# Kernel tuning notes

Hardware: AMD Instinct MI355X
Metric: run time of the kernel (lower is better)

The kernel has to match this reference:

```python
import jax, jax.numpy as jnp
import numpy as np

D_MODEL = 1024
NUM_HEADS = 16
D_K = D_MODEL // NUM_HEADS


def setup_inputs() -> dict:
    key = jax.random.key(0)
    ks = jax.random.split(key, 11)
    B, T = 4, 2048
    s = 1.0 / np.sqrt(D_MODEL)
    return {
        'query': jax.random.normal(ks[0], (B, T, D_MODEL), jnp.float32),
        'key': jax.random.normal(ks[1], (B, T, D_MODEL), jnp.float32),
        'value': jax.random.normal(ks[2], (B, T, D_MODEL), jnp.float32),
        'Wq': jax.random.normal(ks[3], (D_MODEL, D_MODEL), jnp.float32) * s,
        'bq': jnp.zeros((D_MODEL,), jnp.float32),
        'Wk': jax.random.normal(ks[4], (D_MODEL, D_MODEL), jnp.float32) * s,
        'bk': jnp.zeros((D_MODEL,), jnp.float32),
        'Wv': jax.random.normal(ks[5], (D_MODEL, D_MODEL), jnp.float32) * s,
        'bv': jnp.zeros((D_MODEL,), jnp.float32),
        'Wo': jax.random.normal(ks[6], (D_MODEL, D_MODEL), jnp.float32) * s,
        'bo': jnp.zeros((D_MODEL,), jnp.float32),
    }


def reference(query, key, value, Wq, bq, Wk, bk, Wv, bv, Wo, bo):
    B, Tq, _ = query.shape
    Tk = key.shape[1]
    # projections (torch Linear: x @ W.T + b)
    q = (query @ Wq.T + bq).reshape(B, Tq, NUM_HEADS, D_K).transpose(0, 2, 1, 3)
    k = (key @ Wk.T + bk).reshape(B, Tk, NUM_HEADS, D_K).transpose(0, 2, 1, 3)
    v = (value @ Wv.T + bv).reshape(B, Tk, NUM_HEADS, D_K).transpose(0, 2, 1, 3)
    scale = 1.0 / jnp.sqrt(jnp.asarray(D_K, q.dtype))
    scores = jnp.einsum('bhqd,bhkd->bhqk', q, k) * scale  # [B,H,Tq,Tk]
    attn = jax.nn.softmax(scores, axis=-1)
    out = jnp.einsum('bhqk,bhkd->bhqd', attn, v)
    out = out.transpose(0, 2, 1, 3).reshape(B, Tq, D_MODEL)
    return out @ Wo.T + bo
```

## Files before the change

kernel.cpp:

```cpp
#include <hip/hip_runtime.h>

typedef unsigned short u16;
typedef unsigned int u32;
typedef __attribute__((ext_vector_type(8))) short bf16x8;
typedef __attribute__((ext_vector_type(4))) float f32x4;

__device__ inline u16 f2bf(float x) {
  union { float f; unsigned u; } v; v.f = x;
  unsigned r = v.u + 0x7fffu + ((v.u >> 16) & 1u);
  return (u16)(r >> 16);
}

__device__ inline u32 packbf2(float p0, float p1) {
  return __builtin_amdgcn_perm(__float_as_uint(p1), __float_as_uint(p0), 0x07060302u);
}

__device__ inline void gload16(const void* g, void* l) {
  __builtin_amdgcn_global_load_lds(
      (const __attribute__((address_space(1))) unsigned int*)g,
      (__attribute__((address_space(3))) unsigned int*)l,
      16, 0, 0);
}

__global__ void cvt_all(const float* __restrict__ q, const float* __restrict__ k,
                        const float* __restrict__ v,
                        const float* __restrict__ wq, const float* __restrict__ wk,
                        const float* __restrict__ wv, const float* __restrict__ wo,
                        u16* __restrict__ ws) {
  const size_t MT4 = (size_t)2 * 1024 * 1024;
  const int i = blockIdx.x * blockDim.x + threadIdx.x;
  const int t = blockIdx.y;
  float4 vv;
  ushort4 o;
  if (t < 3) {
    const float* src = (t == 0) ? q : (t == 1) ? k : v;
    vv = ((const float4*)src)[i];
    o.x = f2bf(vv.x); o.y = f2bf(vv.y); o.z = f2bf(vv.z); o.w = f2bf(vv.w);
    ((ushort4*)ws)[(size_t)t * MT4 + i] = o;
  } else {
    if (i >= (1 << 20)) return;
    const int w = i >> 18, j = i & 0x3FFFF;
    const float* src = (w == 0) ? wq : (w == 1) ? wk : (w == 2) ? wv : wo;
    vv = ((const float4*)src)[j];
    o.x = f2bf(vv.x); o.y = f2bf(vv.y); o.z = f2bf(vv.z); o.w = f2bf(vv.w);
    ((ushort4*)(ws + 3 * MT4 * 4))[i] = o;
  }
}

__global__ __launch_bounds__(512, 4) void gemm_qkv(
    const u16* __restrict__ Xq, const u16* __restrict__ Wqb,
    const float* __restrict__ bq_, const float* __restrict__ bk_,
    const float* __restrict__ bv_, u16* __restrict__ Qp)
{
  constexpr int N = 1024, K = 1024, BK = 32, NT = K / BK;
  constexpr size_t MT = (size_t)8192 * 1024, WT = (size_t)1024 * 1024;
  __shared__ __align__(16) u16 As[3][128 * BK];
  __shared__ __align__(16) u16 Bs[3][128 * BK];
  const int z = blockIdx.z;
  const u16* A = Xq + (size_t)z * MT;
  const u16* W = Wqb + (size_t)z * WT;
  const float* bias = (z == 0) ? bq_ : (z == 1) ? bk_ : bv_;
  u16* Cout = Qp + (size_t)z * MT;
  const bool vm = (z == 2);

  const int tid = threadIdx.x;
  const int wave = tid >> 6, lane = tid & 63;
  const int quad = lane >> 4, l16 = lane & 15;
  const int m0 = blockIdx.x * 128, n0 = blockIdx.y * 128;

  const int srow = tid >> 2;
  const int sg = ((tid & 3) ^ (srow & 3)) * 8;
  const int arowP = vm ? ((srow & 64) + (srow & 3) * 16 + ((srow & 63) >> 2)) : srow;
  const u16* ag = A + (size_t)(m0 + arowP) * K + sg;
  const u16* bg = W + (size_t)(n0 + srow) * K + sg;

  const int wm = (wave >> 2) * 64, wn = (wave & 3) * 32;
  f32x4 acc[4][2] = {};

#define QKV_STAGE(s)                                   \
  do {                                                 \
    gload16(ag, As[s] + wave * 512);                   \
    gload16(bg, Bs[s] + wave * 512);                   \
    ag += BK; bg += BK;                                \
  } while (0)

  QKV_STAGE(0);
  QKV_STAGE(1);

  int cb = 0, sb = 2;
  for (int kt = 0; kt < NT; ++kt) {
    if (kt + 1 < NT) asm volatile("s_waitcnt vmcnt(2)" ::: "memory");
    else             asm volatile("s_waitcnt vmcnt(0)" ::: "memory");
    __builtin_amdgcn_s_barrier();
    __builtin_amdgcn_sched_barrier(0);
    if (kt + 2 < NT) {
      QKV_STAGE(sb);
      sb = (sb == 2) ? 0 : sb + 1;
    }
    const u16* Ac = As[cb];
    const u16* Bc = Bs[cb];
    cb = (cb == 2) ? 0 : cb + 1;
    bf16x8 af[4], bf[2];
#pragma unroll
    for (int mi = 0; mi < 4; ++mi)
      af[mi] = *(const bf16x8*)(Ac + (wm + mi * 16 + l16) * BK + ((quad ^ (l16 & 3)) * 8));
#pragma unroll
    for (int ni = 0; ni < 2; ++ni)
      bf[ni] = *(const bf16x8*)(Bc + (wn + ni * 16 + l16) * BK + ((quad ^ (l16 & 3)) * 8));
#pragma unroll
    for (int mi = 0; mi < 4; ++mi)
#pragma unroll
      for (int ni = 0; ni < 2; ++ni)
        acc[mi][ni] = __builtin_amdgcn_mfma_f32_16x16x32_bf16(af[mi], bf[ni], acc[mi][ni], 0, 0, 0);
  }
#undef QKV_STAGE

#pragma unroll
  for (int ni = 0; ni < 2; ++ni) {
    const int col = n0 + wn + ni * 16 + l16;
    const float bv = bias[col];
#pragma unroll
    for (int mi = 0; mi < 4; ++mi) {
      const int mrow = m0 + wm + mi * 16 + quad * 4;
      f32x4 a = acc[mi][ni];
      if (!vm) {
#pragma unroll
        for (int r = 0; r < 4; ++r)
          Cout[(size_t)(mrow + r) * N + col] = f2bf(a[r] + bv);
      } else {
        const int bq = mrow >> 11, t = mrow & 2047;
        const int h = col >> 6, d = col & 63;
        ushort4 pk;
        pk.x = f2bf(a[0] + bv); pk.y = f2bf(a[1] + bv);
        pk.z = f2bf(a[2] + bv); pk.w = f2bf(a[3] + bv);
        *(ushort4*)(Cout + ((size_t)((bq * 16 + h) * 64 + d)) * 2048 + t) = pk;
      }
    }
  }
}

__global__ __launch_bounds__(512, 4) void gemm_wo(
    const u16* __restrict__ A, const u16* __restrict__ W,
    const float* __restrict__ bias, float* __restrict__ Cout)
{
  constexpr int N = 1024, K = 1024, BK = 32, NT = K / BK;
  __shared__ __align__(16) u16 As[3][128 * BK];
  __shared__ __align__(16) u16 Bs[3][128 * BK];
  const int tid = threadIdx.x;
  const int wave = tid >> 6, lane = tid & 63;
  const int quad = lane >> 4, l16 = lane & 15;
  const int m0 = blockIdx.x * 128, n0 = blockIdx.y * 128;

  const int srow = tid >> 2;
  const int sg = ((tid & 3) ^ (srow & 3)) * 8;
  const u16* ag = A + (size_t)(m0 + srow) * K + sg;
  const u16* bg = W + (size_t)(n0 + srow) * K + sg;

  const int wm = (wave >> 2) * 64, wn = (wave & 3) * 32;
  f32x4 acc[4][2] = {};

#define WO_STAGE(s)                                    \
  do {                                                 \
    gload16(ag, As[s] + wave * 512);                   \
    gload16(bg, Bs[s] + wave * 512);                   \
    ag += BK; bg += BK;                                \
  } while (0)

  WO_STAGE(0);
  WO_STAGE(1);

  int cb = 0, sb = 2;
  for (int kt = 0; kt < NT; ++kt) {
    if (kt + 1 < NT) asm volatile("s_waitcnt vmcnt(2)" ::: "memory");
    else             asm volatile("s_waitcnt vmcnt(0)" ::: "memory");
    __builtin_amdgcn_s_barrier();
    __builtin_amdgcn_sched_barrier(0);
    if (kt + 2 < NT) {
      WO_STAGE(sb);
      sb = (sb == 2) ? 0 : sb + 1;
    }
    const u16* Ac = As[cb];
    const u16* Bc = Bs[cb];
    cb = (cb == 2) ? 0 : cb + 1;
    bf16x8 af[4], bf[2];
#pragma unroll
    for (int mi = 0; mi < 4; ++mi)
      af[mi] = *(const bf16x8*)(Ac + (wm + mi * 16 + l16) * BK + ((quad ^ (l16 & 3)) * 8));
#pragma unroll
    for (int ni = 0; ni < 2; ++ni)
      bf[ni] = *(const bf16x8*)(Bc + (wn + ni * 16 + l16) * BK + ((quad ^ (l16 & 3)) * 8));
#pragma unroll
    for (int mi = 0; mi < 4; ++mi)
#pragma unroll
      for (int ni = 0; ni < 2; ++ni)
        acc[mi][ni] = __builtin_amdgcn_mfma_f32_16x16x32_bf16(af[mi], bf[ni], acc[mi][ni], 0, 0, 0);
  }
#undef WO_STAGE

#pragma unroll
  for (int ni = 0; ni < 2; ++ni) {
    const int col = n0 + wn + ni * 16 + l16;
    const float bv = bias[col];
#pragma unroll
    for (int mi = 0; mi < 4; ++mi) {
      const int mrow = m0 + wm + mi * 16 + quad * 4;
      f32x4 a = acc[mi][ni];
#pragma unroll
      for (int r = 0; r < 4; ++r)
        Cout[(size_t)(mrow + r) * N + col] = a[r] + bv;
    }
  }
}

__global__ __launch_bounds__(512, 4) void flash_attn(
    const u16* __restrict__ Qp, const u16* __restrict__ Kp,
    const u16* __restrict__ Vt, u16* __restrict__ Ctx)
{
  constexpr int TQ = 2048, DM = 1024, DK = 64;
  __shared__ __align__(16) u16 Ks[2][128 * 64];
  __shared__ __align__(16) u16 Vts[2][64 * 128];
  __shared__ __align__(16) u16 Ps[8][16 * 64];

  const int bh = blockIdx.x, b = bh >> 4, h = bh & 15;
  const int qt = blockIdx.y;
  const int tid = threadIdx.x, wave = tid >> 6, lane = tid & 63;
  const int quad = lane >> 4, l16 = lane & 15;
  const int q0 = qt * 256 + wave * 32;

  const int C0 = tid, C1 = 512 + tid;
  const int kr0 = C0 >> 3, kr1 = C1 >> 3;
  const u16* kp0 = Kp + (size_t)(b * TQ + kr0) * DM + h * DK + (((C0 & 7) ^ (kr0 & 7)) * 8);
  const u16* kp1 = Kp + (size_t)(b * TQ + kr1) * DM + h * DK + (((C1 & 7) ^ (kr1 & 7)) * 8);
  const int vd0 = C0 >> 4, vd1 = C1 >> 4;
  const u16* vp0 = Vt + (size_t)(bh * DK + vd0) * TQ + (((C0 & 15) ^ (vd0 & 15)) * 8);
  const u16* vp1 = Vt + (size_t)(bh * DK + vd1) * TQ + (((C1 & 15) ^ (vd1 & 15)) * 8);

  bf16x8 qf[2][2];
#pragma unroll
  for (int mi = 0; mi < 2; ++mi)
#pragma unroll
    for (int ks = 0; ks < 2; ++ks)
      qf[mi][ks] = *(const bf16x8*)(Qp + (size_t)(b * TQ + q0 + mi * 16 + l16) * DM
                                       + h * DK + ks * 32 + quad * 8);

  f32x4 O[2][4] = {};
  f32x4 lsum[2] = {};
  const float CS = 0.18033688011112042f;
  const float CB = 0.0028153f;

  bf16x8 onesv;
#pragma unroll
  for (int j = 0; j < 8; ++j) onesv[j] = (short)0x3F80;

  gload16(kp0, &Ks[0][C0 * 8]);
  gload16(kp1, &Ks[0][C1 * 8]);
  gload16(vp0, &Vts[0][C0 * 8]);
  gload16(vp1, &Vts[0][C1 * 8]);
  kp0 += 128 * DM; kp1 += 128 * DM; vp0 += 128; vp1 += 128;
  __syncthreads();

  const int kg = quad ^ (l16 & 7);
  int cur = 0;
  for (int kt = 0; kt < TQ / 128; ++kt) {
    if (kt + 1 < TQ / 128) {
      const int nb = cur ^ 1;
      gload16(kp0, &Ks[nb][C0 * 8]);
      gload16(kp1, &Ks[nb][C1 * 8]);
      gload16(vp0, &Vts[nb][C0 * 8]);
      gload16(vp1, &Vts[nb][C1 * 8]);
      kp0 += 128 * DM; kp1 += 128 * DM; vp0 += 128; vp1 += 128;
    }
    const u16* Kc = Ks[cur];
    const u16* Vc = Vts[cur];
    u16* Psw = Ps[wave];

#pragma unroll
    for (int g = 0; g < 2; ++g) {
      f32x4 Sg[2][4];
      __builtin_amdgcn_s_setprio(1);
#pragma unroll
      for (int cc = 0; cc < 4; ++cc) {
        const int row = (g * 4 + cc) * 16 + l16;
        bf16x8 kf0 = *(const bf16x8*)(Kc + row * 64 + kg * 8);
        bf16x8 kf1 = *(const bf16x8*)(Kc + row * 64 + (kg ^ 4) * 8);
#pragma unroll
        for (int mi = 0; mi < 2; ++mi) {
          f32x4 zz = {};
          zz = __builtin_amdgcn_mfma_f32_16x16x32_bf16(qf[mi][0], kf0, zz, 0, 0, 0);
          Sg[mi][cc] = __builtin_amdgcn_mfma_f32_16x16x32_bf16(qf[mi][1], kf1, zz, 0, 0, 0);
        }
      }
      __builtin_amdgcn_s_setprio(0);
      bf16x8 pf[2][2];
#pragma unroll
      for (int mi = 0; mi < 2; ++mi) {
#pragma unroll
        for (int r = 0; r < 4; ++r) {
          float e0 = __builtin_amdgcn_exp2f(fmaf(Sg[mi][0][r], CS, CB));
          float e1 = __builtin_amdgcn_exp2f(fmaf(Sg[mi][1][r], CS, CB));
          float e2 = __builtin_amdgcn_exp2f(fmaf(Sg[mi][2][r], CS, CB));
          float e3 = __builtin_amdgcn_exp2f(fmaf(Sg[mi][3][r], CS, CB));
          uint2 pk;
          pk.x = packbf2(e0, e1);
          pk.y = packbf2(e2, e3);
          const int pw = quad * 4 + r;
          *(uint2*)(&Psw[pw * 64 + ((l16 * 4) ^ ((pw & 7) << 3))]) = pk;
        }
#pragma unroll
        for (int ksl = 0; ksl < 2; ++ksl)
          pf[mi][ksl] = *(const bf16x8*)(&Psw[l16 * 64 + ((ksl * 32 + quad * 8) ^ ((l16 & 7) << 3))]);
#pragma unroll
        for (int ksl = 0; ksl < 2; ++ksl)
          lsum[mi] = __builtin_amdgcn_mfma_f32_16x16x32_bf16(pf[mi][ksl], onesv, lsum[mi], 0, 0, 0);
      }
      __builtin_amdgcn_s_setprio(1);
#pragma unroll
      for (int ksl = 0; ksl < 2; ++ksl)
#pragma unroll
        for (int ni = 0; ni < 4; ++ni) {
          const int gv = g * 8 + ksl * 4 + quad;
          bf16x8 vf = *(const bf16x8*)(Vc + (ni * 16 + l16) * 128 + ((gv ^ l16) * 8));
          O[0][ni] = __builtin_amdgcn_mfma_f32_16x16x32_bf16(pf[0][ksl], vf, O[0][ni], 0, 0, 0);
          O[1][ni] = __builtin_amdgcn_mfma_f32_16x16x32_bf16(pf[1][ksl], vf, O[1][ni], 0, 0, 0);
        }
      __builtin_amdgcn_s_setprio(0);
    }
    __syncthreads();
    cur ^= 1;
  }

#pragma unroll
  for (int mi = 0; mi < 2; ++mi)
#pragma unroll
    for (int r = 0; r < 4; ++r) {
      const float inv = 1.0f / lsum[mi][r];
      const int q = q0 + mi * 16 + quad * 4 + r;
#pragma unroll
      for (int ni = 0; ni < 4; ++ni) {
        const int col = h * DK + ni * 16 + l16;
        Ctx[(size_t)(b * TQ + q) * DM + col] = f2bf(O[mi][ni][r] * inv);
      }
    }
}

extern "C" void kernel_launch(void* const* d_in, const int* in_sizes, int n_in,
                              void* d_out, int out_size, void* d_ws, size_t ws_size,
                              hipStream_t stream)
{
  (void)in_sizes; (void)n_in; (void)out_size; (void)ws_size;
  const float* query = (const float*)d_in[0];
  const float* key_  = (const float*)d_in[1];
  const float* value = (const float*)d_in[2];
  const float* Wq = (const float*)d_in[3];
  const float* bq = (const float*)d_in[4];
  const float* Wk = (const float*)d_in[5];
  const float* bk = (const float*)d_in[6];
  const float* Wv = (const float*)d_in[7];
  const float* bv = (const float*)d_in[8];
  const float* Wo = (const float*)d_in[9];
  const float* bo = (const float*)d_in[10];

  const size_t MT = (size_t)4 * 2048 * 1024;
  const size_t WT = (size_t)1024 * 1024;
  u16* ws  = (u16*)d_ws;
  u16* Xq  = ws;
  u16* Wqb = Xq + 3 * MT;
  u16* Qp  = Wqb + 4 * WT;
  u16* Kp  = Qp + MT;
  u16* Vt  = Kp + MT;
  u16* Ctx = Vt + MT;
  u16* Wob = Wqb + 3 * WT;

  cvt_all<<<dim3(8192, 4), 256, 0, stream>>>(
      query, key_, value, Wq, Wk, Wv, Wo, ws);

  gemm_qkv<<<dim3(64, 8, 3), 512, 0, stream>>>(Xq, Wqb, bq, bk, bv, Qp);

  flash_attn<<<dim3(64, 8), 512, 0, stream>>>(Qp, Kp, Vt, Ctx);

  gemm_wo<<<dim3(64, 8), 512, 0, stream>>>(Ctx, Wob, bo, (float*)d_out);
}
```

Before: 325.0 us.

## Keep softmax probabilities in registers by computing transposed QK^T scores

```diff
diff --git a/kernel.cpp b/kernel.cpp
--- a/kernel.cpp
+++ b/kernel.cpp
@@ -70,7 +70,8 @@
 
   const int srow = tid >> 2;
   const int sg = ((tid & 3) ^ (srow & 3)) * 8;
-  const int arowP = vm ? ((srow & 64) + (srow & 3) * 16 + ((srow & 63) >> 2)) : srow;
+  const int arowP = vm ? ((srow & ~31) | ((srow & 4) << 2) | ((srow & 24) >> 1) | (srow & 3))
+                       : srow;
   const u16* ag = A + (size_t)(m0 + arowP) * K + sg;
   const u16* bg = W + (size_t)(n0 + srow) * K + sg;
 
@@ -219,7 +220,6 @@
   constexpr int TQ = 2048, DM = 1024, DK = 64;
   __shared__ __align__(16) u16 Ks[2][128 * 64];
   __shared__ __align__(16) u16 Vts[2][64 * 128];
-  __shared__ __align__(16) u16 Ps[8][16 * 64];
 
   const int bh = blockIdx.x, b = bh >> 4, h = bh & 15;
   const int qt = blockIdx.y;
@@ -272,7 +272,6 @@
     }
     const u16* Kc = Ks[cur];
     const u16* Vc = Vts[cur];
-    u16* Psw = Ps[wave];
 
 #pragma unroll
     for (int g = 0; g < 2; ++g) {
@@ -286,32 +285,29 @@
 #pragma unroll
         for (int mi = 0; mi < 2; ++mi) {
           f32x4 zz = {};
-          zz = __builtin_amdgcn_mfma_f32_16x16x32_bf16(qf[mi][0], kf0, zz, 0, 0, 0);
-          Sg[mi][cc] = __builtin_amdgcn_mfma_f32_16x16x32_bf16(qf[mi][1], kf1, zz, 0, 0, 0);
+          zz = __builtin_amdgcn_mfma_f32_16x16x32_bf16(kf0, qf[mi][0], zz, 0, 0, 0);
+          Sg[mi][cc] = __builtin_amdgcn_mfma_f32_16x16x32_bf16(kf1, qf[mi][1], zz, 0, 0, 0);
         }
       }
       __builtin_amdgcn_s_setprio(0);
-      bf16x8 pf[2][2];
+      bf16x8 pa[2][2];
 #pragma unroll
       for (int mi = 0; mi < 2; ++mi) {
 #pragma unroll
-        for (int r = 0; r < 4; ++r) {
-          float e0 = __builtin_amdgcn_exp2f(fmaf(Sg[mi][0][r], CS, CB));
-          float e1 = __builtin_amdgcn_exp2f(fmaf(Sg[mi][1][r], CS, CB));
-          float e2 = __builtin_amdgcn_exp2f(fmaf(Sg[mi][2][r], CS, CB));
-          float e3 = __builtin_amdgcn_exp2f(fmaf(Sg[mi][3][r], CS, CB));
-          uint2 pk;
-          pk.x = packbf2(e0, e1);
-          pk.y = packbf2(e2, e3);
-          const int pw = quad * 4 + r;
-          *(uint2*)(&Psw[pw * 64 + ((l16 * 4) ^ ((pw & 7) << 3))]) = pk;
+        for (int ksl = 0; ksl < 2; ++ksl) {
+          uint4 u;
+          u.x = packbf2(__builtin_amdgcn_exp2f(fmaf(Sg[mi][2 * ksl][0], CS, CB)),
+                        __builtin_amdgcn_exp2f(fmaf(Sg[mi][2 * ksl][1], CS, CB)));
+          u.y = packbf2(__builtin_amdgcn_exp2f(fmaf(Sg[mi][2 * ksl][2], CS, CB)),
+                        __builtin_amdgcn_exp2f(fmaf(Sg[mi][2 * ksl][3], CS, CB)));
+          u.z = packbf2(__builtin_amdgcn_exp2f(fmaf(Sg[mi][2 * ksl + 1][0], CS, CB)),
+                        __builtin_amdgcn_exp2f(fmaf(Sg[mi][2 * ksl + 1][1], CS, CB)));
+          u.w = packbf2(__builtin_amdgcn_exp2f(fmaf(Sg[mi][2 * ksl + 1][2], CS, CB)),
+                        __builtin_amdgcn_exp2f(fmaf(Sg[mi][2 * ksl + 1][3], CS, CB)));
+          pa[mi][ksl] = *(const bf16x8*)&u;
         }
-#pragma unroll
-        for (int ksl = 0; ksl < 2; ++ksl)
-          pf[mi][ksl] = *(const bf16x8*)(&Psw[l16 * 64 + ((ksl * 32 + quad * 8) ^ ((l16 & 7) << 3))]);
-#pragma unroll
-        for (int ksl = 0; ksl < 2; ++ksl)
-          lsum[mi] = __builtin_amdgcn_mfma_f32_16x16x32_bf16(pf[mi][ksl], onesv, lsum[mi], 0, 0, 0);
+        lsum[mi] = __builtin_amdgcn_mfma_f32_16x16x32_bf16(pa[mi][0], onesv, lsum[mi], 0, 0, 0);
+        lsum[mi] = __builtin_amdgcn_mfma_f32_16x16x32_bf16(pa[mi][1], onesv, lsum[mi], 0, 0, 0);
       }
       __builtin_amdgcn_s_setprio(1);
 #pragma unroll
@@ -320,8 +316,8 @@
         for (int ni = 0; ni < 4; ++ni) {
           const int gv = g * 8 + ksl * 4 + quad;
           bf16x8 vf = *(const bf16x8*)(Vc + (ni * 16 + l16) * 128 + ((gv ^ l16) * 8));
-          O[0][ni] = __builtin_amdgcn_mfma_f32_16x16x32_bf16(pf[0][ksl], vf, O[0][ni], 0, 0, 0);
-          O[1][ni] = __builtin_amdgcn_mfma_f32_16x16x32_bf16(pf[1][ksl], vf, O[1][ni], 0, 0, 0);
+          O[0][ni] = __builtin_amdgcn_mfma_f32_16x16x32_bf16(pa[0][ksl], vf, O[0][ni], 0, 0, 0);
+          O[1][ni] = __builtin_amdgcn_mfma_f32_16x16x32_bf16(pa[1][ksl], vf, O[1][ni], 0, 0, 0);
         }
       __builtin_amdgcn_s_setprio(0);
     }
```

Result: no change. 325.8 us (+0.2%).
